# Optimization experiments

Measured on AMD Instinct MI355X. Metric: run time of the kernel, lower is better.

Reference implementation:

```python
import jax, jax.numpy as jnp
import numpy as np

B, N, E = 32, 1024, 512   # docs, word-nodes per doc, hyperedges per doc
V = 50001                 # n_node + 1 (padding idx 0)
D = 300                   # initialFeatureSize == n_hid
H = 300                   # hiddenSize (output of gat2)
NEG = -9e15


def _leaky(v, alpha):
    return jnp.where(v > 0, v, alpha * v)


def _hypergat_layer(x, adj, w, w2, w3, a, a2, wc, alpha, concat):
    # x: [B,N,Fin], adj: [B,E,N] 0/1 incidence. Eval mode: dropout = identity.
    Fo = w2.shape[1]
    x4 = x @ w2                                   # [B,N,Fo]
    if w is not None:                             # transfer=True branch
        x = x @ w                                 # [B,N,Fo]
    mask = adj > 0                                # [B,E,N]
    # edge attention: score per node, constant word-context query
    s1 = _leaky(wc @ a[:Fo, 0] + x4 @ a[Fo:, 0], alpha)          # [B,N]
    att_edge = jax.nn.softmax(jnp.where(mask, s1[:, None, :], NEG), axis=2)  # [B,E,N]
    edge = att_edge @ x                           # [B,E,Fo] hyperedge features
    edge4 = edge @ w3                             # [B,E,Fo]
    # node attention: score(node n, edge e) = leaky(x4[n]@a2_top + edge4[e]@a2_bot)
    sc = _leaky((x4 @ a2[:Fo, 0])[:, None, :] + (edge4 @ a2[Fo:, 0])[:, :, None], alpha)  # [B,E,N]
    att_node = jax.nn.softmax(jnp.where(mask, sc, NEG).transpose(0, 2, 1), axis=2)        # [B,N,E]
    node = att_node @ edge                        # [B,N,Fo]
    return jax.nn.elu(node) if concat else node


def setup_inputs() -> dict:
    key = jax.random.key(0)
    ks = jax.random.split(key, 16)
    stdv = 1.0 / np.sqrt(H)  # DocumentGraph.reset_parameters uniform_(-stdv, stdv) on all params
    u = lambda k, shape: jax.random.uniform(k, shape, jnp.float32, -stdv, stdv)
    return dict(
        inputs=jax.random.randint(ks[0], (B, N), 0, V),
        HT=(jax.random.uniform(ks[1], (B, E, N)) < 0.10).astype(jnp.int32),
        emb=u(ks[2], (V, D)),
        w2_1=u(ks[3], (D, D)), w3_1=u(ks[4], (D, D)),
        a_1=u(ks[5], (2 * D, 1)), a2_1=u(ks[6], (2 * D, 1)), wc_1=u(ks[7], (D,)),
        w_2=u(ks[8], (D, H)), w2_2=u(ks[9], (D, H)), w3_2=u(ks[10], (H, H)),
        a_2=u(ks[11], (2 * H, 1)), a2_2=u(ks[12], (2 * H, 1)), wc_2=u(ks[13], (H,)),
    )


def reference(inputs, HT, emb, w2_1, w3_1, a_1, a2_1, wc_1,
              w_2, w2_2, w3_2, a_2, a2_2, wc_2):
    x = emb[inputs]                                # [B,N,D] embedding lookup
    # gat1: transfer=False, concat=True, alpha=0.1
    x = _hypergat_layer(x, HT, None, w2_1, w3_1, a_1, a2_1, wc_1, 0.1, True)
    # gat2: transfer=True, bias=False, concat=False, alpha=0.2
    x = _hypergat_layer(x, HT, w_2, w2_2, w3_2, a_2, a2_2, wc_2, 0.2, False)
    return x
```

## Files before the change

kernel.cpp:

```cpp
#include <hip/hip_runtime.h>
#include <hip/hip_bf16.h>

#define CB 32
#define CN 1024
#define CE 512
#define CD 300
#define EP 320
#define UCAP 320
#define MCAP 192

__global__ void k_embed(const int* __restrict__ idx, const float* __restrict__ emb,
                        float* __restrict__ X) {
    int gid = blockIdx.x * blockDim.x + threadIdx.x;
    const int total = CB * CN * 75;
    if (gid >= total) return;
    int r = gid / 75, c = gid % 75;
    int e = idx[r];
    reinterpret_cast<float4*>(X)[(size_t)r * 75 + c] =
        reinterpret_cast<const float4*>(emb)[(size_t)e * 75 + c];
}

__global__ void k_ebits(const int* __restrict__ HT, unsigned long long* __restrict__ ebits) {
    int gw = (blockIdx.x * blockDim.x + threadIdx.x) >> 6;
    int lane = threadIdx.x & 63;
    const int* hrow = HT + (size_t)gw * CN;
#pragma unroll
    for (int c = 0; c < 16; ++c) {
        unsigned long long bal = __ballot(hrow[(c << 6) + lane] != 0);
        if (lane == 0) ebits[(size_t)gw * 16 + c] = bal;
    }
}

__global__ __launch_bounds__(512) void k_bitT(const unsigned long long* __restrict__ ebits,
        unsigned long long* __restrict__ nbits) {
    __shared__ unsigned long long w[8][64];
    int b = blockIdx.x >> 4, nc = blockIdx.x & 15;
    int tid = threadIdx.x, ec = tid >> 6, lane = tid & 63;
    w[ec][lane] = ebits[((size_t)b * CE + (ec << 6) + lane) * 16 + nc];
    __syncthreads();
    unsigned long long out = 0;
#pragma unroll
    for (int j = 0; j < 64; ++j)
        out |= ((w[ec][j] >> lane) & 1ull) << j;
    nbits[((size_t)b * CN + (nc << 6) + lane) * 8 + ec] = out;
}

__global__ void k_members(const unsigned long long* __restrict__ ebits,
                          unsigned short* __restrict__ mem, int* __restrict__ degs) {
    int gw = (blockIdx.x * blockDim.x + threadIdx.x) >> 6;
    int lane = threadIdx.x & 63;
    const unsigned long long* eb = ebits + (size_t)gw * 16;
    unsigned short* lst = mem + (size_t)gw * MCAP;
    int base = 0;
    unsigned long long lmask = (1ull << lane) - 1ull;
#pragma unroll
    for (int c = 0; c < 16; ++c) {
        unsigned long long w = eb[c];
        if ((w >> lane) & 1ull) {
            int off = base + (int)__popcll(w & lmask);
            if (off < MCAP) lst[off] = (unsigned short)((c << 6) + lane);
        }
        base += (int)__popcll(w);
    }
    if (lane == 0) degs[gw] = base;
}

__global__ void k_prep(const float* __restrict__ w2_1, const float* __restrict__ w3_1,
                       const float* __restrict__ a_1, const float* __restrict__ a2_1,
                       const float* __restrict__ w2_2, const float* __restrict__ w3_2,
                       const float* __restrict__ a_2, const float* __restrict__ a2_2,
                       float* __restrict__ vecs) {
    int which = blockIdx.x;
    int t = threadIdx.x;
    if (t >= CD) return;
    const float* W; const float* v;
    switch (which) {
        case 0:  W = w2_1; v = a_1 + CD;  break;
        case 1:  W = w2_1; v = a2_1;      break;
        case 2:  W = w3_1; v = a2_1 + CD; break;
        case 3:  W = w2_2; v = a_2 + CD;  break;
        case 4:  W = w2_2; v = a2_2;      break;
        default: W = w3_2; v = a2_2 + CD; break;
    }
    float s = 0.f;
    for (int j = 0; j < CD; ++j) s += W[(size_t)t * CD + j] * v[j];
    vecs[which * CD + t] = s;
}

__global__ __launch_bounds__(256) void k_gemm300(const float* __restrict__ A,
                                                 const float* __restrict__ W,
                                                 float* __restrict__ C, int M,
                                                 int lda, int ldc) {
    __shared__ float As[64][20];
    __shared__ float Ws[16][68];
    int tid = threadIdx.x;
    int n0 = blockIdx.x * 64, m0 = blockIdx.y * 64;
    int tx = tid & 15, ty = tid >> 4;
    int la_r = tid >> 2, la_c = (tid & 3) << 2;
    int lw_r = tid >> 4, lw_c = (tid & 15) << 2;
    float acc[4][4] = {};
    for (int k0 = 0; k0 < CD; k0 += 16) {
        {
            int kc = k0 + la_c;
            const float* Ap = A + (size_t)(m0 + la_r) * lda + kc;
            float4 av;
            if (kc + 3 < CD) av = *reinterpret_cast<const float4*>(Ap);
            else {
                av.x = kc     < CD ? Ap[0] : 0.f;
                av.y = kc + 1 < CD ? Ap[1] : 0.f;
                av.z = kc + 2 < CD ? Ap[2] : 0.f;
                av.w = 0.f;
            }
            *reinterpret_cast<float4*>(&As[la_r][la_c]) = av;
        }
        {
            int kr = k0 + lw_r;
            float4 wv = {0.f, 0.f, 0.f, 0.f};
            if (kr < CD) {
                const float* Wp = W + (size_t)kr * CD + n0 + lw_c;
                if (n0 + lw_c + 3 < CD) wv = *reinterpret_cast<const float4*>(Wp);
                else {
                    if (n0 + lw_c     < CD) wv.x = Wp[0];
                    if (n0 + lw_c + 1 < CD) wv.y = Wp[1];
                    if (n0 + lw_c + 2 < CD) wv.z = Wp[2];
                }
            }
            *reinterpret_cast<float4*>(&Ws[lw_r][lw_c]) = wv;
        }
        __syncthreads();
#pragma unroll
        for (int k = 0; k < 16; ++k) {
            float av[4];
#pragma unroll
            for (int i = 0; i < 4; ++i) av[i] = As[ty * 4 + i][k];
            float4 bv = *reinterpret_cast<const float4*>(&Ws[k][tx * 4]);
            float bb[4] = {bv.x, bv.y, bv.z, bv.w};
#pragma unroll
            for (int i = 0; i < 4; ++i)
#pragma unroll
                for (int j = 0; j < 4; ++j) acc[i][j] += av[i] * bb[j];
        }
        __syncthreads();
    }
    for (int i = 0; i < 4; ++i) {
        int m = m0 + ty * 4 + i;
        int n = n0 + tx * 4;
        float* Cp = C + (size_t)m * ldc + n;
        if (n + 3 < CD) {
            float4 v = {acc[i][0], acc[i][1], acc[i][2], acc[i][3]};
            *reinterpret_cast<float4*>(Cp) = v;
        } else {
            for (int j = 0; j < 4; ++j) if (n + j < CD) Cp[j] = acc[i][j];
        }
    }
}

__global__ void k_score(const float* __restrict__ X, const float* __restrict__ av,
                        const float* __restrict__ pv, const float* __restrict__ wc,
                        const float* __restrict__ a_orig,
                        float alpha, float* __restrict__ s1, float* __restrict__ p, int M) {
    int gw = (blockIdx.x * blockDim.x + threadIdx.x) >> 6;
    int lane = threadIdx.x & 63;
    if (gw >= M) return;
    const float* row = X + (size_t)gw * CD;
    float d1 = 0.f, d2 = 0.f, dc = 0.f;
    for (int d = lane; d < CD; d += 64) {
        float x = row[d];
        d1 += x * av[d];
        d2 += x * pv[d];
        dc += wc[d] * a_orig[d];
    }
    for (int o = 32; o; o >>= 1) {
        d1 += __shfl_down(d1, o);
        d2 += __shfl_down(d2, o);
        dc += __shfl_down(dc, o);
    }
    if (lane == 0) {
        float v = dc + d1;
        s1[gw] = v > 0.f ? v : alpha * v;
        p[gw] = d2;
    }
}

__global__ __launch_bounds__(1024) void k_bmax(const float* __restrict__ s1,
                                               float* __restrict__ e1) {
    __shared__ float red[16];
    int b = blockIdx.x, t = threadIdx.x;
    float v = s1[b * CN + t];
    float m = v;
    for (int o = 32; o; o >>= 1) m = fmaxf(m, __shfl_xor(m, o));
    if ((t & 63) == 0) red[t >> 6] = m;
    __syncthreads();
    if (t == 0) {
        float mm = red[0];
        for (int i = 1; i < 16; ++i) mm = fmaxf(mm, red[i]);
        red[0] = mm;
    }
    __syncthreads();
    e1[b * CN + t] = __expf(v - red[0]);
}

__global__ __launch_bounds__(256) void k_edge_agg(const unsigned short* __restrict__ mem,
        const int* __restrict__ degs, const unsigned long long* __restrict__ ebits,
        const float* __restrict__ e1, const float* __restrict__ Xs,
        const float* __restrict__ qvec, float* __restrict__ edge, float* __restrict__ q) {
    int gw = (blockIdx.x * blockDim.x + threadIdx.x) >> 6;
    int lane = threadIdx.x & 63;
    int b = gw >> 9;
    const float* e1b = e1 + b * CN;
    const float* Xb = Xs + (size_t)b * CN * CD;
    int deg = degs[gw];
    float a0 = 0.f, a1 = 0.f, a2 = 0.f, a3 = 0.f, a4 = 0.f;
    float den = 0.f;
    bool tail = lane < (CD - 256);
    if (deg <= MCAP) {
        const unsigned short* lst = mem + (size_t)gw * MCAP;
        int i = 0;
        for (; i + 4 <= deg; i += 4) {
            ushort4 nn = *reinterpret_cast<const ushort4*>(lst + i);
            float w0 = e1b[nn.x], w1 = e1b[nn.y], w2 = e1b[nn.z], w3 = e1b[nn.w];
            const float* r0 = Xb + (size_t)nn.x * CD;
            const float* r1 = Xb + (size_t)nn.y * CD;
            const float* r2 = Xb + (size_t)nn.z * CD;
            const float* r3 = Xb + (size_t)nn.w * CD;
            float v00 = r0[lane], v01 = r0[lane + 64], v02 = r0[lane + 128], v03 = r0[lane + 192];
            float v10 = r1[lane], v11 = r1[lane + 64], v12 = r1[lane + 128], v13 = r1[lane + 192];
            float v20 = r2[lane], v21 = r2[lane + 64], v22 = r2[lane + 128], v23 = r2[lane + 192];
            float v30 = r3[lane], v31 = r3[lane + 64], v32 = r3[lane + 128], v33 = r3[lane + 192];
            float v04 = 0.f, v14 = 0.f, v24 = 0.f, v34 = 0.f;
            if (tail) { v04 = r0[lane + 256]; v14 = r1[lane + 256]; v24 = r2[lane + 256]; v34 = r3[lane + 256]; }
            den += w0; den += w1; den += w2; den += w3;
            a0 += w0 * v00; a0 += w1 * v10; a0 += w2 * v20; a0 += w3 * v30;
            a1 += w0 * v01; a1 += w1 * v11; a1 += w2 * v21; a1 += w3 * v31;
            a2 += w0 * v02; a2 += w1 * v12; a2 += w2 * v22; a2 += w3 * v32;
            a3 += w0 * v03; a3 += w1 * v13; a3 += w2 * v23; a3 += w3 * v33;
            a4 += w0 * v04; a4 += w1 * v14; a4 += w2 * v24; a4 += w3 * v34;
        }
        for (; i < deg; ++i) {
            int n = lst[i];
            float w = e1b[n];
            const float* r = Xb + (size_t)n * CD;
            den += w;
            a0 += w * r[lane];
            a1 += w * r[lane + 64];
            a2 += w * r[lane + 128];
            a3 += w * r[lane + 192];
            if (tail) a4 += w * r[lane + 256];
        }
    } else {
        const unsigned long long* eb = ebits + (size_t)gw * 16;
#pragma unroll
        for (int c = 0; c < 16; ++c) {
            int n0 = c << 6;
            float wv = e1b[n0 + lane];
            unsigned long long bal = eb[c];
            while (bal) {
                int jj = (int)__ffsll(bal) - 1;
                bal &= bal - 1ull;
                float w = __shfl(wv, jj);
                const float* row = Xb + (size_t)(n0 + jj) * CD;
                den += w;
                a0 += w * row[lane];
                a1 += w * row[lane + 64];
                a2 += w * row[lane + 128];
                a3 += w * row[lane + 192];
                if (tail) a4 += w * row[lane + 256];
            }
        }
    }
    float inv = deg > 0 ? 1.f / den : 0.f;
    float o0 = a0 * inv, o1 = a1 * inv, o2 = a2 * inv, o3 = a3 * inv;
    float o4 = tail ? a4 * inv : 0.f;
    float* erow = edge + (size_t)gw * EP;
    erow[lane]       = o0;
    erow[lane + 64]  = o1;
    erow[lane + 128] = o2;
    erow[lane + 192] = o3;
    erow[lane + 256] = o4;
    float d2 = o0 * qvec[lane];
    d2 += o1 * qvec[lane + 64];
    d2 += o2 * qvec[lane + 128];
    d2 += o3 * qvec[lane + 192];
    if (tail) d2 += o4 * qvec[lane + 256];
    for (int o = 32; o; o >>= 1) d2 += __shfl_down(d2, o);
    if (lane == 0) q[gw] = d2;
}

#define ACC16(vv, ww) do { \
    acc[0][0] += (ww).x * (vv).x; acc[0][1] += (ww).x * (vv).y; \
    acc[0][2] += (ww).x * (vv).z; acc[0][3] += (ww).x * (vv).w; \
    acc[1][0] += (ww).y * (vv).x; acc[1][1] += (ww).y * (vv).y; \
    acc[1][2] += (ww).y * (vv).z; acc[1][3] += (ww).y * (vv).w; \
    acc[2][0] += (ww).z * (vv).x; acc[2][1] += (ww).z * (vv).y; \
    acc[2][2] += (ww).z * (vv).z; acc[2][3] += (ww).z * (vv).w; \
    acc[3][0] += (ww).w * (vv).x; acc[3][1] += (ww).w * (vv).y; \
    acc[3][2] += (ww).w * (vv).z; acc[3][3] += (ww).w * (vv).w; \
} while (0)

__global__ __launch_bounds__(320) void k_node_attn(const unsigned long long* __restrict__ nbits,
        const float* __restrict__ p, const float* __restrict__ q,
        const float* __restrict__ edge, float alpha, int do_elu, float* __restrict__ out) {
    __shared__ float4 wsc[4][UCAP];
    __shared__ __align__(8) unsigned short ul[4][UCAP];
    __shared__ int ucnt_s[4], flag_s[4];
    __shared__ float gpn[16], gmx[16], gsc[16];
    __shared__ int gct[16];
    int blk = blockIdx.x;
    int b = blk >> 6, n0 = (blk & 63) << 4;
    int tid = threadIdx.x, wv = tid >> 6, lane = tid & 63;
    const float* qb = q + b * CE;

    if (wv < 4) {
        float pn[4]; const unsigned long long* nb[4];
#pragma unroll
        for (int k = 0; k < 4; ++k) {
            int n = n0 + 4 * wv + k;
            pn[k] = p[b * CN + n];
            nb[k] = nbits + ((size_t)b * CN + n) * 8;
        }
        float sc[4][8];
        int cnt[4] = {0, 0, 0, 0};
        float mx[4] = {-3.4e38f, -3.4e38f, -3.4e38f, -3.4e38f};
        int ubits = 0;
#pragma unroll
        for (int j = 0; j < 8; ++j) {
            int e = lane + (j << 6);
            float qe = qb[e];
            int many = 0;
#pragma unroll
            for (int k = 0; k < 4; ++k) {
                int m = (int)((nb[k][j] >> lane) & 1ull);
                float v = pn[k] + qe;
                v = v > 0.f ? v : alpha * v;
                v = m ? v : -3.0e38f;
                cnt[k] += m; many |= m;
                mx[k] = fmaxf(mx[k], v);
                sc[k][j] = v;
            }
            ubits |= (many ? 1 : 0) << j;
        }
#pragma unroll
        for (int k = 0; k < 4; ++k) {
            for (int o = 32; o; o >>= 1) {
                mx[k] = fmaxf(mx[k], __shfl_xor(mx[k], o));
                cnt[k] += __shfl_xor(cnt[k], o);
            }
        }
        float scale[4];
#pragma unroll
        for (int k = 0; k < 4; ++k) {
            float s = 0.f;
#pragma unroll
            for (int j = 0; j < 8; ++j) { float w8 = __expf(sc[k][j] - mx[k]); sc[k][j] = w8; s += w8; }
            for (int o = 32; o; o >>= 1) s += __shfl_xor(s, o);
            scale[k] = cnt[k] > 0 ? 1.f / s : 1.f;
        }
        int base = 0;
        unsigned long long lmask = (1ull << lane) - 1ull;
#pragma unroll
        for (int j = 0; j < 8; ++j) {
            unsigned long long bal = __ballot((ubits >> j) & 1);
            if ((ubits >> j) & 1) {
                int off = base + (int)__popcll(bal & lmask);
                if (off < UCAP) {
                    ul[wv][off] = (unsigned short)(lane + (j << 6));
                    wsc[wv][off] = make_float4(sc[0][j] * scale[0], sc[1][j] * scale[1],
                                               sc[2][j] * scale[2], sc[3][j] * scale[3]);
                }
            }
            base += (int)__popcll(bal);
        }
        if (lane == 0) {
            ucnt_s[wv] = base < UCAP ? base : UCAP;
            flag_s[wv] = (cnt[0] == 0) | (cnt[1] == 0) | (cnt[2] == 0) | (cnt[3] == 0) |
                         (base > UCAP);
            gpn[wv*4+0]=pn[0]; gmx[wv*4+0]=mx[0]; gsc[wv*4+0]=scale[0]; gct[wv*4+0]=cnt[0];
            gpn[wv*4+1]=pn[1]; gmx[wv*4+1]=mx[1]; gsc[wv*4+1]=scale[1]; gct[wv*4+1]=cnt[1];
            gpn[wv*4+2]=pn[2]; gmx[wv*4+2]=mx[2]; gsc[wv*4+2]=scale[2]; gct[wv*4+2]=cnt[2];
            gpn[wv*4+3]=pn[3]; gmx[wv*4+3]=mx[3]; gsc[wv*4+3]=scale[3]; gct[wv*4+3]=cnt[3];
        }
    }
    __syncthreads();

    int grp = tid / 80;
    int j4 = tid - grp * 80;
    const float4* eb4 = reinterpret_cast<const float4*>(edge + (size_t)b * CE * EP) + j4;
    int cnt = ucnt_s[grp], bad = flag_s[grp];
    float acc[4][4] = {};
    if (!bad) {
        int i = 0;
        for (; i + 8 <= cnt; i += 8) {
            ushort4 ua = *reinterpret_cast<const ushort4*>(&ul[grp][i]);
            ushort4 ub = *reinterpret_cast<const ushort4*>(&ul[grp][i + 4]);
            float4 v0 = eb4[(size_t)ua.x * 80], v1 = eb4[(size_t)ua.y * 80];
            float4 v2 = eb4[(size_t)ua.z * 80], v3 = eb4[(size_t)ua.w * 80];
            float4 v4 = eb4[(size_t)ub.x * 80], v5 = eb4[(size_t)ub.y * 80];
            float4 v6 = eb4[(size_t)ub.z * 80], v7 = eb4[(size_t)ub.w * 80];
            { float4 w = wsc[grp][i];     ACC16(v0, w); }
            { float4 w = wsc[grp][i + 1]; ACC16(v1, w); }
            { float4 w = wsc[grp][i + 2]; ACC16(v2, w); }
            { float4 w = wsc[grp][i + 3]; ACC16(v3, w); }
            { float4 w = wsc[grp][i + 4]; ACC16(v4, w); }
            { float4 w = wsc[grp][i + 5]; ACC16(v5, w); }
            { float4 w = wsc[grp][i + 6]; ACC16(v6, w); }
            { float4 w = wsc[grp][i + 7]; ACC16(v7, w); }
        }
        for (; i < cnt; ++i) {
            int e = ul[grp][i];
            float4 v = eb4[(size_t)e * 80];
            float4 w = wsc[grp][i];
            ACC16(v, w);
        }
    } else {
        float pnk[4], mxk[4], sck[4]; int ctk[4];
        const unsigned long long* nbr[4];
#pragma unroll
        for (int k = 0; k < 4; ++k) {
            pnk[k] = gpn[grp*4+k]; mxk[k] = gmx[grp*4+k]; sck[k] = gsc[grp*4+k]; ctk[k] = gct[grp*4+k];
            nbr[k] = nbits + ((size_t)b * CN + n0 + grp * 4 + k) * 8;
        }
        for (int e = 0; e < CE; ++e) {
            float4 v = eb4[(size_t)e * 80];
            float qe = qb[e];
#pragma unroll
            for (int k = 0; k < 4; ++k) {
                int m = (int)((nbr[k][e >> 6] >> (e & 63)) & 1ull);
                float vv = pnk[k] + qe; vv = vv > 0.f ? vv : alpha * vv;
                float w = ctk[k] == 0 ? (1.f / CE) : (m ? __expf(vv - mxk[k]) * sck[k] : 0.f);
                acc[k][0] += w * v.x; acc[k][1] += w * v.y; acc[k][2] += w * v.z; acc[k][3] += w * v.w;
            }
        }
    }
    if (j4 < 75) {
#pragma unroll
        for (int ni = 0; ni < 4; ++ni) {
            float4 o = {acc[ni][0], acc[ni][1], acc[ni][2], acc[ni][3]};
            if (do_elu) {
                o.x = o.x > 0.f ? o.x : expm1f(o.x);
                o.y = o.y > 0.f ? o.y : expm1f(o.y);
                o.z = o.z > 0.f ? o.z : expm1f(o.z);
                o.w = o.w > 0.f ? o.w : expm1f(o.w);
            }
            *reinterpret_cast<float4*>(out + ((size_t)b * CN + n0 + grp * 4 + ni) * CD + j4 * 4) = o;
        }
    }
}

extern "C" void kernel_launch(void* const* d_in, const int* in_sizes, int n_in,
                              void* d_out, int out_size, void* d_ws, size_t ws_size,
                              hipStream_t stream) {
    const int*   inputs = (const int*)d_in[0];
    const int*   HT     = (const int*)d_in[1];
    const float* emb    = (const float*)d_in[2];
    const float* w2_1   = (const float*)d_in[3];
    const float* w3_1   = (const float*)d_in[4];
    const float* a_1    = (const float*)d_in[5];
    const float* a2_1   = (const float*)d_in[6];
    const float* wc_1   = (const float*)d_in[7];
    const float* w_2    = (const float*)d_in[8];
    const float* w2_2   = (const float*)d_in[9];
    const float* w3_2   = (const float*)d_in[10];
    const float* a_2    = (const float*)d_in[11];
    const float* a2_2   = (const float*)d_in[12];
    const float* wc_2   = (const float*)d_in[13];

    char* ws = (char*)d_ws;
    float* big0               = (float*)(ws);
    float* big1               = (float*)(ws + 39321600);
    float* edge               = (float*)(ws + 78643200);
    unsigned long long* ebits = (unsigned long long*)(ws + 99614720);
    unsigned long long* nbits = (unsigned long long*)(ws + 101711872);
    unsigned short* mem       = (unsigned short*)(ws + 103809024);
    int* degs                 = (int*)(ws + 110100480);
    float* s1                 = (float*)(ws + 110166016);
    float* p                  = (float*)(ws + 110297088);
    float* e1                 = (float*)(ws + 110428160);
    float* qv                 = (float*)(ws + 110559232);
    float* vecs               = (float*)(ws + 110624768);

    k_embed<<<9600, 256, 0, stream>>>(inputs, emb, big0);
    k_ebits<<<4096, 256, 0, stream>>>(HT, ebits);
    k_bitT<<<512, 512, 0, stream>>>(ebits, nbits);
    k_members<<<4096, 256, 0, stream>>>(ebits, mem, degs);
    k_prep<<<6, 320, 0, stream>>>(w2_1, w3_1, a_1, a2_1, w2_2, w3_2, a_2, a2_2, vecs);

    k_score<<<CB * CN / 4, 256, 0, stream>>>(big0, vecs, vecs + CD, wc_1, a_1, 0.1f, s1, p, CB * CN);
    k_bmax<<<CB, 1024, 0, stream>>>(s1, e1);
    k_edge_agg<<<4096, 256, 0, stream>>>(mem, degs, ebits, e1, big0, vecs + 2 * CD, edge, qv);
    k_node_attn<<<2048, 320, 0, stream>>>(nbits, p, qv, edge, 0.1f, 1, big0);

    k_score<<<CB * CN / 4, 256, 0, stream>>>(big0, vecs + 3 * CD, vecs + 4 * CD, wc_2, a_2, 0.2f, s1, p, CB * CN);
    k_gemm300<<<dim3(5, 512), 256, 0, stream>>>(big0, w_2, big1, CB * CN, CD, CD);
    k_bmax<<<CB, 1024, 0, stream>>>(s1, e1);
    k_edge_agg<<<4096, 256, 0, stream>>>(mem, degs, ebits, e1, big1, vecs + 5 * CD, edge, qv);
    k_node_attn<<<2048, 320, 0, stream>>>(nbits, p, qv, edge, 0.2f, 0, (float*)d_out);
}
```

Measured before the change: 651.7 us.

## Map one wavefront per node in node attention using precomputed per-node edge lists

```diff
diff --git a/kernel.cpp b/kernel.cpp
--- a/kernel.cpp
+++ b/kernel.cpp
@@ -6,8 +6,8 @@
 #define CE 512
 #define CD 300
 #define EP 320
-#define UCAP 320
 #define MCAP 192
+#define NCAP 96
 
 __global__ void k_embed(const int* __restrict__ idx, const float* __restrict__ emb,
                         float* __restrict__ X) {
@@ -63,6 +63,26 @@
         base += (int)__popcll(w);
     }
     if (lane == 0) degs[gw] = base;
+}
+
+__global__ void k_nmem(const unsigned long long* __restrict__ nbits,
+                       unsigned short* __restrict__ nmem, int* __restrict__ ndegs) {
+    int row = (blockIdx.x * blockDim.x + threadIdx.x) >> 6;
+    int lane = threadIdx.x & 63;
+    const unsigned long long* nb = nbits + (size_t)row * 8;
+    unsigned short* lst = nmem + (size_t)row * NCAP;
+    int base = 0;
+    unsigned long long lmask = (1ull << lane) - 1ull;
+#pragma unroll
+    for (int c = 0; c < 8; ++c) {
+        unsigned long long w = nb[c];
+        if ((w >> lane) & 1ull) {
+            int off = base + (int)__popcll(w & lmask);
+            if (off < NCAP) lst[off] = (unsigned short)((c << 6) + lane);
+        }
+        base += (int)__popcll(w);
+    }
+    if (lane == 0) ndegs[row] = base;
 }
 
 __global__ void k_prep(const float* __restrict__ w2_1, const float* __restrict__ w3_1,
@@ -286,164 +306,114 @@
     if (lane == 0) q[gw] = d2;
 }
 
-#define ACC16(vv, ww) do { \
-    acc[0][0] += (ww).x * (vv).x; acc[0][1] += (ww).x * (vv).y; \
-    acc[0][2] += (ww).x * (vv).z; acc[0][3] += (ww).x * (vv).w; \
-    acc[1][0] += (ww).y * (vv).x; acc[1][1] += (ww).y * (vv).y; \
-    acc[1][2] += (ww).y * (vv).z; acc[1][3] += (ww).y * (vv).w; \
-    acc[2][0] += (ww).z * (vv).x; acc[2][1] += (ww).z * (vv).y; \
-    acc[2][2] += (ww).z * (vv).z; acc[2][3] += (ww).z * (vv).w; \
-    acc[3][0] += (ww).w * (vv).x; acc[3][1] += (ww).w * (vv).y; \
-    acc[3][2] += (ww).w * (vv).z; acc[3][3] += (ww).w * (vv).w; \
-} while (0)
-
-__global__ __launch_bounds__(320) void k_node_attn(const unsigned long long* __restrict__ nbits,
+__global__ __launch_bounds__(512, 8) void k_node_attn(
+        const unsigned long long* __restrict__ nbits,
+        const unsigned short* __restrict__ nmem, const int* __restrict__ ndegs,
         const float* __restrict__ p, const float* __restrict__ q,
-        const float* __restrict__ edge, float alpha, int do_elu, float* __restrict__ out) {
-    __shared__ float4 wsc[4][UCAP];
-    __shared__ __align__(8) unsigned short ul[4][UCAP];
-    __shared__ int ucnt_s[4], flag_s[4];
-    __shared__ float gpn[16], gmx[16], gsc[16];
-    __shared__ int gct[16];
-    int blk = blockIdx.x;
-    int b = blk >> 6, n0 = (blk & 63) << 4;
-    int tid = threadIdx.x, wv = tid >> 6, lane = tid & 63;
-    const float* qb = q + b * CE;
-
-    if (wv < 4) {
-        float pn[4]; const unsigned long long* nb[4];
-#pragma unroll
-        for (int k = 0; k < 4; ++k) {
-            int n = n0 + 4 * wv + k;
-            pn[k] = p[b * CN + n];
-            nb[k] = nbits + ((size_t)b * CN + n) * 8;
-        }
-        float sc[4][8];
-        int cnt[4] = {0, 0, 0, 0};
-        float mx[4] = {-3.4e38f, -3.4e38f, -3.4e38f, -3.4e38f};
-        int ubits = 0;
-#pragma unroll
-        for (int j = 0; j < 8; ++j) {
-            int e = lane + (j << 6);
-            float qe = qb[e];
-            int many = 0;
-#pragma unroll
-            for (int k = 0; k < 4; ++k) {
-                int m = (int)((nb[k][j] >> lane) & 1ull);
-                float v = pn[k] + qe;
-                v = v > 0.f ? v : alpha * v;
-                v = m ? v : -3.0e38f;
-                cnt[k] += m; many |= m;
-                mx[k] = fmaxf(mx[k], v);
-                sc[k][j] = v;
-            }
-            ubits |= (many ? 1 : 0) << j;
-        }
-#pragma unroll
-        for (int k = 0; k < 4; ++k) {
-            for (int o = 32; o; o >>= 1) {
-                mx[k] = fmaxf(mx[k], __shfl_xor(mx[k], o));
-                cnt[k] += __shfl_xor(cnt[k], o);
-            }
-        }
-        float scale[4];
-#pragma unroll
-        for (int k = 0; k < 4; ++k) {
-            float s = 0.f;
-#pragma unroll
-            for (int j = 0; j < 8; ++j) { float w8 = __expf(sc[k][j] - mx[k]); sc[k][j] = w8; s += w8; }
-            for (int o = 32; o; o >>= 1) s += __shfl_xor(s, o);
-            scale[k] = cnt[k] > 0 ? 1.f / s : 1.f;
-        }
-        int base = 0;
-        unsigned long long lmask = (1ull << lane) - 1ull;
-#pragma unroll
-        for (int j = 0; j < 8; ++j) {
-            unsigned long long bal = __ballot((ubits >> j) & 1);
-            if ((ubits >> j) & 1) {
-                int off = base + (int)__popcll(bal & lmask);
-                if (off < UCAP) {
-                    ul[wv][off] = (unsigned short)(lane + (j << 6));
-                    wsc[wv][off] = make_float4(sc[0][j] * scale[0], sc[1][j] * scale[1],
-                                               sc[2][j] * scale[2], sc[3][j] * scale[3]);
-                }
-            }
-            base += (int)__popcll(bal);
-        }
-        if (lane == 0) {
-            ucnt_s[wv] = base < UCAP ? base : UCAP;
-            flag_s[wv] = (cnt[0] == 0) | (cnt[1] == 0) | (cnt[2] == 0) | (cnt[3] == 0) |
-                         (base > UCAP);
-            gpn[wv*4+0]=pn[0]; gmx[wv*4+0]=mx[0]; gsc[wv*4+0]=scale[0]; gct[wv*4+0]=cnt[0];
-            gpn[wv*4+1]=pn[1]; gmx[wv*4+1]=mx[1]; gsc[wv*4+1]=scale[1]; gct[wv*4+1]=cnt[1];
-            gpn[wv*4+2]=pn[2]; gmx[wv*4+2]=mx[2]; gsc[wv*4+2]=scale[2]; gct[wv*4+2]=cnt[2];
-            gpn[wv*4+3]=pn[3]; gmx[wv*4+3]=mx[3]; gsc[wv*4+3]=scale[3]; gct[wv*4+3]=cnt[3];
-        }
-    }
-    __syncthreads();
-
-    int grp = tid / 80;
-    int j4 = tid - grp * 80;
-    const float4* eb4 = reinterpret_cast<const float4*>(edge + (size_t)b * CE * EP) + j4;
-    int cnt = ucnt_s[grp], bad = flag_s[grp];
-    float acc[4][4] = {};
-    if (!bad) {
+        const float* __restrict__ edge, float alpha, int do_elu,
+        float* __restrict__ out) {
+    __shared__ float ws[8][CE];
+    int wv = threadIdx.x >> 6, lane = threadIdx.x & 63;
+    int node = blockIdx.x * 8 + wv;
+    int b = node >> 10;
+    const float* qb = q + (size_t)b * CE;
+    const unsigned long long* nb = nbits + (size_t)node * 8;
+
+    float pn = p[node];
+    float sc[8];
+    int cnt = 0;
+    float mx = -3.4e38f;
+#pragma unroll
+    for (int j = 0; j < 8; ++j) {
+        int m = (int)((nb[j] >> lane) & 1ull);
+        float v = pn + qb[(j << 6) + lane];
+        v = v > 0.f ? v : alpha * v;
+        v = m ? v : -3.0e38f;
+        sc[j] = v;
+        cnt += m;
+        mx = fmaxf(mx, v);
+    }
+    for (int o = 32; o; o >>= 1) {
+        mx = fmaxf(mx, __shfl_xor(mx, o));
+        cnt += __shfl_xor(cnt, o);
+    }
+    float s = 0.f;
+#pragma unroll
+    for (int j = 0; j < 8; ++j) { float w = __expf(sc[j] - mx); sc[j] = w; s += w; }
+    for (int o = 32; o; o >>= 1) s += __shfl_xor(s, o);
+    float scale = cnt > 0 ? 1.f / s : 1.f;
+#pragma unroll
+    for (int j = 0; j < 8; ++j) {
+        int m = (int)((nb[j] >> lane) & 1ull);
+        ws[wv][(j << 6) + lane] = m ? sc[j] * scale : 0.f;
+    }
+
+    const float4* eb4 = reinterpret_cast<const float4*>(edge + (size_t)b * CE * EP);
+    bool two = lane < 11;
+    float4 acc0 = {0.f, 0.f, 0.f, 0.f}, acc1 = {0.f, 0.f, 0.f, 0.f};
+    int deg = ndegs[node];
+    if (cnt > 0 && deg <= NCAP) {
+        const unsigned short* lst = nmem + (size_t)node * NCAP;
         int i = 0;
-        for (; i + 8 <= cnt; i += 8) {
-            ushort4 ua = *reinterpret_cast<const ushort4*>(&ul[grp][i]);
-            ushort4 ub = *reinterpret_cast<const ushort4*>(&ul[grp][i + 4]);
-            float4 v0 = eb4[(size_t)ua.x * 80], v1 = eb4[(size_t)ua.y * 80];
-            float4 v2 = eb4[(size_t)ua.z * 80], v3 = eb4[(size_t)ua.w * 80];
-            float4 v4 = eb4[(size_t)ub.x * 80], v5 = eb4[(size_t)ub.y * 80];
-            float4 v6 = eb4[(size_t)ub.z * 80], v7 = eb4[(size_t)ub.w * 80];
-            { float4 w = wsc[grp][i];     ACC16(v0, w); }
-            { float4 w = wsc[grp][i + 1]; ACC16(v1, w); }
-            { float4 w = wsc[grp][i + 2]; ACC16(v2, w); }
-            { float4 w = wsc[grp][i + 3]; ACC16(v3, w); }
-            { float4 w = wsc[grp][i + 4]; ACC16(v4, w); }
-            { float4 w = wsc[grp][i + 5]; ACC16(v5, w); }
-            { float4 w = wsc[grp][i + 6]; ACC16(v6, w); }
-            { float4 w = wsc[grp][i + 7]; ACC16(v7, w); }
-        }
-        for (; i < cnt; ++i) {
-            int e = ul[grp][i];
-            float4 v = eb4[(size_t)e * 80];
-            float4 w = wsc[grp][i];
-            ACC16(v, w);
+        for (; i + 4 <= deg; i += 4) {
+            ushort4 ee = *reinterpret_cast<const ushort4*>(lst + i);
+            float w0 = ws[wv][ee.x], w1 = ws[wv][ee.y];
+            float w2 = ws[wv][ee.z], w3 = ws[wv][ee.w];
+            const float4* r0 = eb4 + (size_t)ee.x * 80;
+            const float4* r1 = eb4 + (size_t)ee.y * 80;
+            const float4* r2 = eb4 + (size_t)ee.z * 80;
+            const float4* r3 = eb4 + (size_t)ee.w * 80;
+            float4 v0 = r0[lane], v1 = r1[lane], v2 = r2[lane], v3 = r3[lane];
+            float4 u0, u1, u2, u3;
+            if (two) { u0 = r0[64 + lane]; u1 = r1[64 + lane]; u2 = r2[64 + lane]; u3 = r3[64 + lane]; }
+            acc0.x += w0 * v0.x; acc0.y += w0 * v0.y; acc0.z += w0 * v0.z; acc0.w += w0 * v0.w;
+            acc0.x += w1 * v1.x; acc0.y += w1 * v1.y; acc0.z += w1 * v1.z; acc0.w += w1 * v1.w;
+            acc0.x += w2 * v2.x; acc0.y += w2 * v2.y; acc0.z += w2 * v2.z; acc0.w += w2 * v2.w;
+            acc0.x += w3 * v3.x; acc0.y += w3 * v3.y; acc0.z += w3 * v3.z; acc0.w += w3 * v3.w;
+            if (two) {
+                acc1.x += w0 * u0.x; acc1.y += w0 * u0.y; acc1.z += w0 * u0.z; acc1.w += w0 * u0.w;
+                acc1.x += w1 * u1.x; acc1.y += w1 * u1.y; acc1.z += w1 * u1.z; acc1.w += w1 * u1.w;
+                acc1.x += w2 * u2.x; acc1.y += w2 * u2.y; acc1.z += w2 * u2.z; acc1.w += w2 * u2.w;
+                acc1.x += w3 * u3.x; acc1.y += w3 * u3.y; acc1.z += w3 * u3.z; acc1.w += w3 * u3.w;
+            }
+        }
+        for (; i < deg; ++i) {
+            int e = lst[i];
+            float w = ws[wv][e];
+            const float4* r = eb4 + (size_t)e * 80;
+            float4 v = r[lane];
+            acc0.x += w * v.x; acc0.y += w * v.y; acc0.z += w * v.z; acc0.w += w * v.w;
+            if (two) {
+                float4 u = r[64 + lane];
+                acc1.x += w * u.x; acc1.y += w * u.y; acc1.z += w * u.z; acc1.w += w * u.w;
+            }
         }
     } else {
-        float pnk[4], mxk[4], sck[4]; int ctk[4];
-        const unsigned long long* nbr[4];
-#pragma unroll
-        for (int k = 0; k < 4; ++k) {
-            pnk[k] = gpn[grp*4+k]; mxk[k] = gmx[grp*4+k]; sck[k] = gsc[grp*4+k]; ctk[k] = gct[grp*4+k];
-            nbr[k] = nbits + ((size_t)b * CN + n0 + grp * 4 + k) * 8;
-        }
+        float uw = 1.f / (float)CE;
         for (int e = 0; e < CE; ++e) {
-            float4 v = eb4[(size_t)e * 80];
-            float qe = qb[e];
-#pragma unroll
-            for (int k = 0; k < 4; ++k) {
-                int m = (int)((nbr[k][e >> 6] >> (e & 63)) & 1ull);
-                float vv = pnk[k] + qe; vv = vv > 0.f ? vv : alpha * vv;
-                float w = ctk[k] == 0 ? (1.f / CE) : (m ? __expf(vv - mxk[k]) * sck[k] : 0.f);
-                acc[k][0] += w * v.x; acc[k][1] += w * v.y; acc[k][2] += w * v.z; acc[k][3] += w * v.w;
-            }
-        }
-    }
-    if (j4 < 75) {
-#pragma unroll
-        for (int ni = 0; ni < 4; ++ni) {
-            float4 o = {acc[ni][0], acc[ni][1], acc[ni][2], acc[ni][3]};
-            if (do_elu) {
-                o.x = o.x > 0.f ? o.x : expm1f(o.x);
-                o.y = o.y > 0.f ? o.y : expm1f(o.y);
-                o.z = o.z > 0.f ? o.z : expm1f(o.z);
-                o.w = o.w > 0.f ? o.w : expm1f(o.w);
-            }
-            *reinterpret_cast<float4*>(out + ((size_t)b * CN + n0 + grp * 4 + ni) * CD + j4 * 4) = o;
-        }
-    }
+            float w = cnt > 0 ? ws[wv][e] : uw;
+            const float4* r = eb4 + (size_t)e * 80;
+            float4 v = r[lane];
+            acc0.x += w * v.x; acc0.y += w * v.y; acc0.z += w * v.z; acc0.w += w * v.w;
+            if (two) {
+                float4 u = r[64 + lane];
+                acc1.x += w * u.x; acc1.y += w * u.y; acc1.z += w * u.z; acc1.w += w * u.w;
+            }
+        }
+    }
+    if (do_elu) {
+        acc0.x = acc0.x > 0.f ? acc0.x : expm1f(acc0.x);
+        acc0.y = acc0.y > 0.f ? acc0.y : expm1f(acc0.y);
+        acc0.z = acc0.z > 0.f ? acc0.z : expm1f(acc0.z);
+        acc0.w = acc0.w > 0.f ? acc0.w : expm1f(acc0.w);
+        acc1.x = acc1.x > 0.f ? acc1.x : expm1f(acc1.x);
+        acc1.y = acc1.y > 0.f ? acc1.y : expm1f(acc1.y);
+        acc1.z = acc1.z > 0.f ? acc1.z : expm1f(acc1.z);
+        acc1.w = acc1.w > 0.f ? acc1.w : expm1f(acc1.w);
+    }
+    float* orow = out + (size_t)node * CD;
+    *reinterpret_cast<float4*>(orow + (lane << 2)) = acc0;
+    if (two) *reinterpret_cast<float4*>(orow + ((64 + lane) << 2)) = acc1;
 }
 
 extern "C" void kernel_launch(void* const* d_in, const int* in_sizes, int n_in,
@@ -471,27 +441,30 @@
     unsigned long long* ebits = (unsigned long long*)(ws + 99614720);
     unsigned long long* nbits = (unsigned long long*)(ws + 101711872);
     unsigned short* mem       = (unsigned short*)(ws + 103809024);
-    int* degs                 = (int*)(ws + 110100480);
-    float* s1                 = (float*)(ws + 110166016);
-    float* p                  = (float*)(ws + 110297088);
-    float* e1                 = (float*)(ws + 110428160);
-    float* qv                 = (float*)(ws + 110559232);
-    float* vecs               = (float*)(ws + 110624768);
+    unsigned short* nmem      = (unsigned short*)(ws + 110100480);
+    int* degs                 = (int*)(ws + 116391936);
+    int* ndegs                = (int*)(ws + 116457472);
+    float* s1                 = (float*)(ws + 116588544);
+    float* p                  = (float*)(ws + 116719616);
+    float* e1                 = (float*)(ws + 116850688);
+    float* qv                 = (float*)(ws + 116981760);
+    float* vecs               = (float*)(ws + 117047296);
 
     k_embed<<<9600, 256, 0, stream>>>(inputs, emb, big0);
     k_ebits<<<4096, 256, 0, stream>>>(HT, ebits);
     k_bitT<<<512, 512, 0, stream>>>(ebits, nbits);
     k_members<<<4096, 256, 0, stream>>>(ebits, mem, degs);
+    k_nmem<<<8192, 256, 0, stream>>>(nbits, nmem, ndegs);
     k_prep<<<6, 320, 0, stream>>>(w2_1, w3_1, a_1, a2_1, w2_2, w3_2, a_2, a2_2, vecs);
 
     k_score<<<CB * CN / 4, 256, 0, stream>>>(big0, vecs, vecs + CD, wc_1, a_1, 0.1f, s1, p, CB * CN);
     k_bmax<<<CB, 1024, 0, stream>>>(s1, e1);
     k_edge_agg<<<4096, 256, 0, stream>>>(mem, degs, ebits, e1, big0, vecs + 2 * CD, edge, qv);
-    k_node_attn<<<2048, 320, 0, stream>>>(nbits, p, qv, edge, 0.1f, 1, big0);
+    k_node_attn<<<4096, 512, 0, stream>>>(nbits, nmem, ndegs, p, qv, edge, 0.1f, 1, big0);
 
     k_score<<<CB * CN / 4, 256, 0, stream>>>(big0, vecs + 3 * CD, vecs + 4 * CD, wc_2, a_2, 0.2f, s1, p, CB * CN);
     k_gemm300<<<dim3(5, 512), 256, 0, stream>>>(big0, w_2, big1, CB * CN, CD, CD);
     k_bmax<<<CB, 1024, 0, stream>>>(s1, e1);
     k_edge_agg<<<4096, 256, 0, stream>>>(mem, degs, ebits, e1, big1, vecs + 5 * CD, edge, qv);
-    k_node_attn<<<2048, 320, 0, stream>>>(nbits, p, qv, edge, 0.2f, 0, (float*)d_out);
-}
+    k_node_attn<<<4096, 512, 0, stream>>>(nbits, nmem, ndegs, p, qv, edge, 0.2f, 0, (float*)d_out);
+}
```

New measurement: 704.5 us. +8.1%, slower.
